# Performance work log

Measured on AMD Instinct MI355X. Metric: run time of the kernel, lower is better.

Reference implementation:

```python
import jax, jax.numpy as jnp
import numpy as np

HEADS = 16
HEAD_DIM = 64
TOKEN_DIM = 1024
INNER = HEADS * HEAD_DIM


def setup_inputs() -> dict:
    key = jax.random.key(0)
    k1, k2, k3, k4 = jax.random.split(key, 4)
    x = jax.random.normal(k1, (2, 2048, TOKEN_DIM), dtype=jnp.float32)
    # nn.Linear(token_dim, inner*3, bias=False): weight [3*inner, token_dim]
    w_qkv = jax.random.normal(k2, (3 * INNER, TOKEN_DIM), dtype=jnp.float32) * (TOKEN_DIM ** -0.5)
    # nn.Linear(inner, token_dim): weight [token_dim, inner], bias [token_dim]
    w_out = jax.random.normal(k3, (TOKEN_DIM, INNER), dtype=jnp.float32) * (INNER ** -0.5)
    b_out = jax.random.normal(k4, (TOKEN_DIM,), dtype=jnp.float32) * 0.01
    return {"x": x, "w_qkv": w_qkv, "w_out": w_out, "b_out": b_out}


def reference(x, w_qkv, w_out, b_out):
    b, n, _ = x.shape
    scale = HEAD_DIM ** -0.5
    qkv = x @ w_qkv.T                                  # [b, n, 3*inner]
    q, k, v = jnp.split(qkv, 3, axis=-1)
    def split_heads(t):
        return t.reshape(b, n, HEADS, HEAD_DIM).transpose(0, 2, 1, 3)  # [b,h,n,d]
    q, k, v = split_heads(q), split_heads(k), split_heads(v)
    dot = jnp.einsum('bhtd,bhsd->bhts', q, k) * scale  # [b,h,n,n]
    attn = jax.nn.softmax(dot, axis=-1)
    out = jnp.einsum('bhts,bhsd->bhtd', attn, v)       # [b,h,n,d]
    out = out.transpose(0, 2, 1, 3).reshape(b, n, INNER)
    return out @ w_out.T + b_out
```

## Files before the change

### kernel.cpp

```cpp
#include <hip/hip_runtime.h>
#include <hip/hip_bf16.h>

typedef short short4v __attribute__((ext_vector_type(4)));
typedef short short8 __attribute__((ext_vector_type(8)));
typedef float float4v __attribute__((ext_vector_type(4)));

#define HEADS 16
#define HDIM 64
#define TOKDIM 1024
#define SEQ 2048
#define BATCH 2
#define BH (BATCH*HEADS)
#define MROWS (BATCH*SEQ)

__device__ __forceinline__ short f2b(float f) {
    __hip_bfloat16 h = __float2bfloat16(f);
    return *reinterpret_cast<short*>(&h);
}
__device__ __forceinline__ float b2f(short s) {
    __hip_bfloat16 h;
    *reinterpret_cast<short*>(&h) = s;
    return __bfloat162float(h);
}
__device__ __forceinline__ short8 load8_f32_bf16(const float* __restrict__ p) {
    float4v a = *(const float4v*)p;
    float4v b = *(const float4v*)(p + 4);
    short8 r;
    r[0]=f2b(a[0]); r[1]=f2b(a[1]); r[2]=f2b(a[2]); r[3]=f2b(a[3]);
    r[4]=f2b(b[0]); r[5]=f2b(b[1]); r[6]=f2b(b[2]); r[7]=f2b(b[3]);
    return r;
}
__device__ __forceinline__ int packrn(float a, float b) {
    unsigned ua = __float_as_uint(a) + 0x8000u;
    unsigned ub = __float_as_uint(b) + 0x8000u;
    return (int)__builtin_amdgcn_perm(ub, ua, 0x07060302u);
}
__device__ __forceinline__ float hexp2(float x) {
    return __builtin_amdgcn_exp2f(x);
}

__device__ __forceinline__ void stage16(const void* g, void* l) {
    __builtin_amdgcn_global_load_lds((const __attribute__((address_space(1))) void*)g,
                                     (__attribute__((address_space(3))) void*)l, 16, 0, 0);
}

__global__ __launch_bounds__(256)
void cvt_bf16(const float* __restrict__ x,  short* __restrict__ xb,  int n8x,
              const float* __restrict__ wq, short* __restrict__ wqb, int n8q,
              const float* __restrict__ wo, short* __restrict__ wob, int n8o)
{
    int i = blockIdx.x*256 + threadIdx.x;
    const float* s; short* d; int off;
    if (i < n8x)                  { s = x;  d = xb;  off = i; }
    else if (i < n8x + n8q)       { s = wq; d = wqb; off = i - n8x; }
    else if (i < n8x + n8q + n8o) { s = wo; d = wob; off = i - n8x - n8q; }
    else return;
    *(short8*)&d[(size_t)off*8] = load8_f32_bf16(&s[(size_t)off*8]);
}

template<int ABF16>
__global__ __launch_bounds__(256)
void gemm_qkv(const void* __restrict__ Ap, const short* __restrict__ Wq,
              short* __restrict__ Qo, short* __restrict__ Ko, short* __restrict__ Vto)
{
    __shared__ __align__(16) short As[128*32];
    __shared__ __align__(16) short Bs[128*32];
    const int tid  = threadIdx.x;
    const int lane = tid & 63;
    const int wave = tid >> 6;
    const int wm = wave >> 1, wn = wave & 1;
    const int m0 = blockIdx.x * 128;
    const int n0 = blockIdx.y * 128;
    const int col16 = lane & 15, quad = lane >> 4;

    const int srow = lane >> 2;
    const int scol = (lane & 3) * 8;

    float4v acc[4][4];
    #pragma unroll
    for (int i=0;i<4;i++)
        #pragma unroll
        for (int j=0;j<4;j++) acc[i][j] = (float4v){0.f,0.f,0.f,0.f};

    for (int k0 = 0; k0 < TOKDIM; k0 += 32) {
        __syncthreads();
        if (ABF16) {
            const short* A = (const short*)Ap;
            #pragma unroll
            for (int j=0;j<2;++j) {
                const int rb = (wave*2 + j) * 16;
                stage16(&A[(size_t)(m0 + rb + srow)*TOKDIM + k0 + scol], &As[rb*32]);
            }
        } else {
            const float* A = (const float*)Ap;
            #pragma unroll
            for (int s=0;s<2;++s) {
                int blk = tid + s*256;
                int r = blk >> 2, kb = blk & 3;
                *(short8*)&As[r*32 + kb*8] = load8_f32_bf16(&A[(size_t)(m0+r)*TOKDIM + k0 + kb*8]);
            }
        }
        #pragma unroll
        for (int j=0;j<2;++j) {
            const int rb = (wave*2 + j) * 16;
            stage16(&Wq[(size_t)(n0 + rb + srow)*TOKDIM + k0 + scol], &Bs[rb*32]);
        }
        __syncthreads();

        short8 af[4], bfr[4];
        #pragma unroll
        for (int i=0;i<4;i++) af[i]  = *(const short8*)&As[(wm*64 + i*16 + col16)*32 + quad*8];
        #pragma unroll
        for (int j=0;j<4;j++) bfr[j] = *(const short8*)&Bs[(wn*64 + j*16 + col16)*32 + quad*8];
        #pragma unroll
        for (int i=0;i<4;i++)
            #pragma unroll
            for (int j=0;j<4;j++)
                acc[i][j] = __builtin_amdgcn_mfma_f32_16x16x32_bf16(af[i], bfr[j], acc[i][j], 0,0,0);
    }

    #pragma unroll
    for (int i=0;i<4;i++)
        #pragma unroll
        for (int j=0;j<4;j++) {
            const int n = n0 + wn*64 + j*16 + col16;
            const int part = n >> 10;
            const int h = (n & 1023) >> 6;
            const int d = n & 63;
            const int mb = m0 + wm*64 + i*16 + quad*4;
            const int b = mb >> 11;
            const int t = mb & 2047;
            if (part == 2) {
                union { short4v s; int2 i2; } w;
                #pragma unroll
                for (int r=0;r<4;r++) w.s[r] = f2b(acc[i][j][r]);
                *(int2*)&Vto[((size_t)(b*HEADS + h)*HDIM + d)*SEQ + t] = w.i2;
            } else {
                short* dst = (part == 0) ? Qo : Ko;
                #pragma unroll
                for (int r=0;r<4;r++)
                    dst[((size_t)(b*HEADS + h)*SEQ + t + r)*HDIM + d] = f2b(acc[i][j][r]);
            }
        }
}

__global__ __launch_bounds__(256)
void gemm_out(const short* __restrict__ A, const short* __restrict__ W,
              const float* __restrict__ bias, float* __restrict__ C)
{
    __shared__ __align__(16) short As[64*32];
    __shared__ __align__(16) short Bs[128*32];
    const int tid  = threadIdx.x;
    const int lane = tid & 63;
    const int wave = tid >> 6;
    const int wm = wave >> 1, wn = wave & 1;
    const int m0 = blockIdx.x * 64;
    const int n0 = blockIdx.y * 128;
    const int col16 = lane & 15, quad = lane >> 4;

    const int srow = lane >> 2;
    const int scol = (lane & 3) * 8;

    float4v acc[2][4];
    #pragma unroll
    for (int i=0;i<2;i++)
        #pragma unroll
        for (int j=0;j<4;j++) acc[i][j] = (float4v){0.f,0.f,0.f,0.f};

    for (int k0 = 0; k0 < TOKDIM; k0 += 32) {
        __syncthreads();
        {
            const int rb = wave * 16;
            stage16(&A[(size_t)(m0 + rb + srow)*TOKDIM + k0 + scol], &As[rb*32]);
        }
        #pragma unroll
        for (int j=0;j<2;++j) {
            const int rb = (wave*2 + j) * 16;
            stage16(&W[(size_t)(n0 + rb + srow)*TOKDIM + k0 + scol], &Bs[rb*32]);
        }
        __syncthreads();

        short8 af[2], bfr[4];
        #pragma unroll
        for (int i=0;i<2;i++) af[i]  = *(const short8*)&As[(wm*32 + i*16 + col16)*32 + quad*8];
        #pragma unroll
        for (int j=0;j<4;j++) bfr[j] = *(const short8*)&Bs[(wn*64 + j*16 + col16)*32 + quad*8];
        #pragma unroll
        for (int i=0;i<2;i++)
            #pragma unroll
            for (int j=0;j<4;j++)
                acc[i][j] = __builtin_amdgcn_mfma_f32_16x16x32_bf16(af[i], bfr[j], acc[i][j], 0,0,0);
    }

    #pragma unroll
    for (int i=0;i<2;i++)
        #pragma unroll
        for (int j=0;j<4;j++) {
            const int n = n0 + wn*64 + j*16 + col16;
            const float bn = bias[n];
            #pragma unroll
            for (int r=0;r<4;r++) {
                const int m = m0 + wm*32 + i*16 + quad*4 + r;
                C[(size_t)m*TOKDIM + n] = acc[i][j][r] + bn;
            }
        }
}

#define AQB 128
#define KT  64
#define NTH 16
#define KVT (KT*HDIM)
#define BUF2 (2*KVT)

__global__ __launch_bounds__(256, 2)
void attn_kernel(const short* __restrict__ Q, const short* __restrict__ K,
                 const short* __restrict__ Vt, short* __restrict__ AO)
{
    __shared__ __align__(16) short SL[2*2*BUF2];

    const int tid   = threadIdx.x;
    const int lane  = tid & 63;
    const int wave  = tid >> 6;
    const int col16 = lane & 15, quad = lane >> 4;
    const int bh  = blockIdx.y;
    const int qh  = wave & 1;
    const int kh2 = wave >> 1;
    const int qb  = blockIdx.x*AQB + qh*64;

    const short* Qb = Q  + (size_t)bh*SEQ*HDIM;
    const short* Kb = K  + (size_t)bh*SEQ*HDIM;
    const short* Vb = Vt + (size_t)bh*HDIM*SEQ;

    short* Sbase = &SL[kh2*2*BUF2];
    const int kbase = kh2 * 1024;

    const int w   = wave & 1;
    const int l3  = lane >> 3;
    const int scsw = (((lane & 7) ^ l3) << 4) >> 1;
    int krow[4], vrow[4];
    #pragma unroll
    for (int c=0;c<4;++c) {
        const int s = w*32 + c*8 + l3;
        krow[c] = (s&32) + ((s&12)<<1) + ((s&16)>>2) + (s&3);
        vrow[c] = s;
    }

    const int r7 = col16 & 7;
    int scol2[2];
    #pragma unroll
    for (int j=0;j<2;++j)
        scol2[j] = ((((j<<6) | (quad<<4)) ^ (r7<<4)) >> 1);

    const float qscale = 0.125f * 1.44269504088896f;
    short8 qf[4][2];
    #pragma unroll
    for (int qg=0; qg<4; ++qg)
        #pragma unroll
        for (int kk=0; kk<2; ++kk) {
            short8 raw = *(const short8*)&Qb[(size_t)(qb+qg*16+col16)*HDIM + kk*32 + quad*8];
            #pragma unroll
            for (int j=0;j<8;++j) raw[j] = f2b(b2f(raw[j]) * qscale);
            qf[qg][kk] = raw;
        }

    const short one_bf16 = (short)0x3F80;
    const short8 vones = {one_bf16, one_bf16, one_bf16, one_bf16,
                          one_bf16, one_bf16, one_bf16, one_bf16};

    float4v o[4][4];
    float4v o1[4];
    #pragma unroll
    for (int qg=0;qg<4;qg++) {
        #pragma unroll
        for (int dt=0;dt<4;dt++) o[qg][dt] = (float4v){0.f,0.f,0.f,0.f};
        o1[qg] = (float4v){0.f,0.f,0.f,0.f};
    }

    {
        short* Kn = Sbase;
        short* Vn = Sbase + KVT;
        #pragma unroll
        for (int c=0;c<4;++c) {
            stage16(&Kb[(size_t)(kbase + krow[c])*HDIM + scsw], &Kn[w*2048 + c*512]);
            stage16(&Vb[(size_t)vrow[c]*SEQ + kbase + scsw],    &Vn[w*2048 + c*512]);
        }
    }
    __syncthreads();

    for (int t = 0; t < NTH; ++t) {
        short* Kc = Sbase + (t & 1)*BUF2;
        short* Vc = Kc + KVT;

        if (t + 1 < NTH) {
            const int g1 = kbase + (t+1)*KT;
            short* Kn = Sbase + ((t & 1)^1)*BUF2;
            short* Vn = Kn + KVT;
            #pragma unroll
            for (int c=0;c<4;++c) {
                stage16(&Kb[(size_t)(g1 + krow[c])*HDIM + scsw], &Kn[w*2048 + c*512]);
                stage16(&Vb[(size_t)vrow[c]*SEQ + g1 + scsw],    &Vn[w*2048 + c*512]);
            }
        }

        #pragma unroll
        for (int kk = 0; kk < 2; ++kk) {
            short8 ka[2][2];
            #pragma unroll
            for (int nt=0; nt<2; ++nt)
                #pragma unroll
                for (int kh=0; kh<2; ++kh)
                    ka[nt][kh] = *(const short8*)&Kc[(kk*32 + nt*16 + col16)*64 + scol2[kh]];
            short8 va[4];
            #pragma unroll
            for (int dt=0; dt<4; ++dt)
                va[dt] = *(const short8*)&Vc[(dt*16 + col16)*64 + scol2[kk]];

            #pragma unroll
            for (int qg=0; qg<4; ++qg) {
                float4v st[2];
                __builtin_amdgcn_s_setprio(1);
                #pragma unroll
                for (int nt=0; nt<2; ++nt) {
                    float4v z = (float4v){0.f,0.f,0.f,0.f};
                    z = __builtin_amdgcn_mfma_f32_16x16x32_bf16(ka[nt][0], qf[qg][0], z, 0,0,0);
                    z = __builtin_amdgcn_mfma_f32_16x16x32_bf16(ka[nt][1], qf[qg][1], z, 0,0,0);
                    st[nt] = z;
                }
                __builtin_amdgcn_s_setprio(0);
                union { int i[4]; short8 s8; } pb;
                float p00 = hexp2(st[0][0]), p01 = hexp2(st[0][1]);
                float p02 = hexp2(st[0][2]), p03 = hexp2(st[0][3]);
                float p10 = hexp2(st[1][0]), p11 = hexp2(st[1][1]);
                float p12 = hexp2(st[1][2]), p13 = hexp2(st[1][3]);
                pb.i[0] = packrn(p00, p01); pb.i[1] = packrn(p02, p03);
                pb.i[2] = packrn(p10, p11); pb.i[3] = packrn(p12, p13);

                __builtin_amdgcn_s_setprio(1);
                #pragma unroll
                for (int dt=0; dt<4; ++dt)
                    o[qg][dt] = __builtin_amdgcn_mfma_f32_16x16x32_bf16(va[dt], pb.s8, o[qg][dt], 0,0,0);
                o1[qg] = __builtin_amdgcn_mfma_f32_16x16x32_bf16(vones, pb.s8, o1[qg], 0,0,0);
                __builtin_amdgcn_s_setprio(0);
            }
        }

        __syncthreads();
    }

    float lsum[4];
    #pragma unroll
    for (int qg=0; qg<4; ++qg) lsum[qg] = o1[qg][0];

    float* M = (float*)SL;
    float* Mw = M + (qh*64 + lane)*68;
    if (kh2 == 1) {
        #pragma unroll
        for (int qg=0; qg<4; ++qg) {
            #pragma unroll
            for (int dt=0; dt<4; ++dt)
                *(float4v*)&Mw[(qg*4+dt)*4] = o[qg][dt];
            Mw[64+qg] = lsum[qg];
        }
    }
    __syncthreads();
    if (kh2 == 0) {
        const int b = bh >> 4, h = bh & 15;
        #pragma unroll
        for (int qg=0; qg<4; ++qg) {
            lsum[qg] += Mw[64+qg];
            const float inv = 1.0f / lsum[qg];
            const int tq = qb + qg*16 + col16;
            #pragma unroll
            for (int dt=0; dt<4; ++dt) {
                float4v ov = o[qg][dt] + *(const float4v*)&Mw[(qg*4+dt)*4];
                union { short4v s; int2 i2; } w2;
                #pragma unroll
                for (int r=0;r<4;++r) w2.s[r] = f2b(ov[r] * inv);
                *(int2*)&AO[((size_t)(b*SEQ + tq))*TOKDIM + h*64 + dt*16 + quad*4] = w2.i2;
            }
        }
    }
}

extern "C" void kernel_launch(void* const* d_in, const int* in_sizes, int n_in,
                              void* d_out, int out_size, void* d_ws, size_t ws_size,
                              hipStream_t stream)
{
    const float* x    = (const float*)d_in[0];
    const float* wqkv = (const float*)d_in[1];
    const float* wout = (const float*)d_in[2];
    const float* bout = (const float*)d_in[3];
    float* out = (float*)d_out;

    char* ws = (char*)d_ws;
    const size_t SZ   = (size_t)BH*SEQ*HDIM*sizeof(short);
    const size_t WQB  = (size_t)3*TOKDIM*TOKDIM*sizeof(short);
    const size_t WOB  = (size_t)TOKDIM*TOKDIM*sizeof(short);
    const size_t NEED_FULL = SZ + WQB + WOB + 3*SZ;
    const bool full = ws_size >= NEED_FULL;

    short *Xb, *Wqb, *Wob, *Qt, *Kt, *Vt, *AO;
    if (full) {
        Xb  = (short*)ws;
        Wqb = (short*)(ws + SZ);
        Wob = (short*)(ws + SZ + WQB);
        Qt  = (short*)(ws + SZ + WQB + WOB);
        Kt  = Qt + SZ/2;
        Vt  = Kt + SZ/2;
        AO  = Xb;
    } else {
        Xb  = nullptr;
        Wqb = (short*)ws;
        Wob = (short*)(ws + WQB);
        Qt  = (short*)(ws + WQB + WOB);
        Kt  = Qt + SZ/2;
        Vt  = Kt + SZ/2;
        AO  = Vt + SZ/2;
    }

    const int n8x = full ? (BATCH*SEQ*TOKDIM)/8 : 0;
    const int n8q = (3*TOKDIM*TOKDIM)/8;
    const int n8o = (TOKDIM*TOKDIM)/8;
    const int cvt_blocks = (n8x + n8q + n8o + 255) / 256;
    cvt_bf16<<<cvt_blocks, 256, 0, stream>>>(x, Xb, n8x, wqkv, Wqb, n8q, wout, Wob, n8o);

    if (full)
        gemm_qkv<1><<<dim3(MROWS/128, (3*TOKDIM)/128), 256, 0, stream>>>(
            (const void*)Xb, Wqb, Qt, Kt, Vt);
    else
        gemm_qkv<0><<<dim3(MROWS/128, (3*TOKDIM)/128), 256, 0, stream>>>(
            (const void*)x, Wqb, Qt, Kt, Vt);

    attn_kernel<<<dim3(SEQ/AQB, BH), 256, 0, stream>>>(Qt, Kt, Vt, AO);

    gemm_out<<<dim3(MROWS/64, TOKDIM/128), 256, 0, stream>>>(AO, Wob, bout, out);
}
```

Before: 171.9 us.

## Add 256x256 double-buffered swizzled QKV GEMM with 512 threads

Replaces the 128x128, BK=32 QKV projection GEMM on the bf16 path with a 256x256 tile, BK=64 kernel using 8 waves. It double-buffers LDS so global-to-LDS loads for the next K tile overlap MFMA work, and uses an XOR swizzle to avoid LDS bank conflicts. It also raises wave priority around MFMA. The larger tile improves operand reuse, but the grid drops to 16x12=192 blocks, which may underfill the CUs, and 128KB of LDS per block limits occupancy.

```diff
diff --git a/kernel.cpp b/kernel.cpp
--- a/kernel.cpp
+++ b/kernel.cpp
@@ -58,10 +58,115 @@
     *(short8*)&d[(size_t)off*8] = load8_f32_bf16(&s[(size_t)off*8]);
 }
 
-template<int ABF16>
+#define GBM 256
+#define GBN 256
+#define GBK 64
+#define GKT (TOKDIM/GBK)
+
+__global__ __launch_bounds__(512)
+void gemm_qkv_big(const short* __restrict__ A, const short* __restrict__ Wq,
+                  short* __restrict__ Qo, short* __restrict__ Ko, short* __restrict__ Vto)
+{
+    __shared__ __align__(16) short Asl[2*GBM*GBK];
+    __shared__ __align__(16) short Bsl[2*GBN*GBK];
+
+    const int tid  = threadIdx.x;
+    const int lane = tid & 63;
+    const int wv   = tid >> 6;
+    const int wm   = wv >> 2;
+    const int wn   = wv & 3;
+    const int col16 = lane & 15, quad = lane >> 4;
+    const int m0 = blockIdx.x * GBM;
+    const int n0 = blockIdx.y * GBN;
+
+    const int srow   = lane >> 3;
+    const int scol   = (((lane & 7) ^ srow) << 3);
+
+    const int r7 = col16 & 7;
+    const int rdoff0 = (((0*4) + quad) ^ r7) << 3;
+    const int rdoff1 = (((1*4) + quad) ^ r7) << 3;
+
+    float4v acc[8][4];
+    #pragma unroll
+    for (int m=0;m<8;m++)
+        #pragma unroll
+        for (int j=0;j<4;j++) acc[m][j] = (float4v){0.f,0.f,0.f,0.f};
+
+    #pragma unroll
+    for (int c=0;c<4;++c) {
+        const int rb = (wv*4 + c)*8;
+        stage16(&A [(size_t)(m0 + rb + srow)*TOKDIM + scol], &Asl[rb*GBK]);
+        stage16(&Wq[(size_t)(n0 + rb + srow)*TOKDIM + scol], &Bsl[rb*GBK]);
+    }
+    asm volatile("s_waitcnt vmcnt(0)" ::: "memory");
+    __builtin_amdgcn_s_barrier();
+
+    for (int kt = 0; kt < GKT; ++kt) {
+        const int buf = kt & 1;
+        const short* Ab = &Asl[buf*GBM*GBK];
+        const short* Bb = &Bsl[buf*GBN*GBK];
+        short* An = &Asl[(buf^1)*GBM*GBK];
+        short* Bn = &Bsl[(buf^1)*GBN*GBK];
+        const bool more = (kt + 1 < GKT);
+        const int k1 = (kt + 1)*GBK;
+
+        #pragma unroll
+        for (int p = 0; p < 4; ++p) {
+            if (more) {
+                const int rb = (wv*4 + p)*8;
+                stage16(&A [(size_t)(m0 + rb + srow)*TOKDIM + k1 + scol], &An[rb*GBK]);
+                stage16(&Wq[(size_t)(n0 + rb + srow)*TOKDIM + k1 + scol], &Bn[rb*GBK]);
+            }
+            const int mh = p >> 1, kk = p & 1;
+            const int rdoff = kk ? rdoff1 : rdoff0;
+            short8 af[4], bfr[4];
+            #pragma unroll
+            for (int i=0;i<4;i++)
+                af[i]  = *(const short8*)&Ab[(wm*128 + mh*64 + i*16 + col16)*GBK + rdoff];
+            #pragma unroll
+            for (int j=0;j<4;j++)
+                bfr[j] = *(const short8*)&Bb[(wn*64 + j*16 + col16)*GBK + rdoff];
+            __builtin_amdgcn_s_setprio(1);
+            #pragma unroll
+            for (int i=0;i<4;i++)
+                #pragma unroll
+                for (int j=0;j<4;j++)
+                    acc[mh*4+i][j] = __builtin_amdgcn_mfma_f32_16x16x32_bf16(af[i], bfr[j], acc[mh*4+i][j], 0,0,0);
+            __builtin_amdgcn_s_setprio(0);
+        }
+
+        asm volatile("s_waitcnt vmcnt(0)" ::: "memory");
+        __builtin_amdgcn_s_barrier();
+    }
+
+    #pragma unroll
+    for (int m=0;m<8;m++)
+        #pragma unroll
+        for (int j=0;j<4;j++) {
+            const int n = n0 + wn*64 + j*16 + col16;
+            const int part = n >> 10;
+            const int h = (n & 1023) >> 6;
+            const int d = n & 63;
+            const int mb = m0 + wm*128 + m*16 + quad*4;
+            const int b = mb >> 11;
+            const int t = mb & 2047;
+            if (part == 2) {
+                union { short4v s; int2 i2; } w;
+                #pragma unroll
+                for (int r=0;r<4;r++) w.s[r] = f2b(acc[m][j][r]);
+                *(int2*)&Vto[((size_t)(b*HEADS + h)*HDIM + d)*SEQ + t] = w.i2;
+            } else {
+                short* dst = (part == 0) ? Qo : Ko;
+                #pragma unroll
+                for (int r=0;r<4;r++)
+                    dst[((size_t)(b*HEADS + h)*SEQ + t + r)*HDIM + d] = f2b(acc[m][j][r]);
+            }
+        }
+}
+
 __global__ __launch_bounds__(256)
-void gemm_qkv(const void* __restrict__ Ap, const short* __restrict__ Wq,
-              short* __restrict__ Qo, short* __restrict__ Ko, short* __restrict__ Vto)
+void gemm_qkv_small(const float* __restrict__ A, const short* __restrict__ Wq,
+                    short* __restrict__ Qo, short* __restrict__ Ko, short* __restrict__ Vto)
 {
     __shared__ __align__(16) short As[128*32];
     __shared__ __align__(16) short Bs[128*32];
@@ -84,21 +189,11 @@
 
     for (int k0 = 0; k0 < TOKDIM; k0 += 32) {
         __syncthreads();
-        if (ABF16) {
-            const short* A = (const short*)Ap;
-            #pragma unroll
-            for (int j=0;j<2;++j) {
-                const int rb = (wave*2 + j) * 16;
-                stage16(&A[(size_t)(m0 + rb + srow)*TOKDIM + k0 + scol], &As[rb*32]);
-            }
-        } else {
-            const float* A = (const float*)Ap;
-            #pragma unroll
-            for (int s=0;s<2;++s) {
-                int blk = tid + s*256;
-                int r = blk >> 2, kb = blk & 3;
-                *(short8*)&As[r*32 + kb*8] = load8_f32_bf16(&A[(size_t)(m0+r)*TOKDIM + k0 + kb*8]);
-            }
+        #pragma unroll
+        for (int s=0;s<2;++s) {
+            int blk = tid + s*256;
+            int r = blk >> 2, kb = blk & 3;
+            *(short8*)&As[r*32 + kb*8] = load8_f32_bf16(&A[(size_t)(m0+r)*TOKDIM + k0 + kb*8]);
         }
         #pragma unroll
         for (int j=0;j<2;++j) {
@@ -425,11 +520,11 @@
     cvt_bf16<<<cvt_blocks, 256, 0, stream>>>(x, Xb, n8x, wqkv, Wqb, n8q, wout, Wob, n8o);
 
     if (full)
-        gemm_qkv<1><<<dim3(MROWS/128, (3*TOKDIM)/128), 256, 0, stream>>>(
-            (const void*)Xb, Wqb, Qt, Kt, Vt);
+        gemm_qkv_big<<<dim3(MROWS/GBM, (3*TOKDIM)/GBN), 512, 0, stream>>>(
+            Xb, Wqb, Qt, Kt, Vt);
     else
-        gemm_qkv<0><<<dim3(MROWS/128, (3*TOKDIM)/128), 256, 0, stream>>>(
-            (const void*)x, Wqb, Qt, Kt, Vt);
+        gemm_qkv_small<<<dim3(MROWS/128, (3*TOKDIM)/128), 256, 0, stream>>>(
+            x, Wqb, Qt, Kt, Vt);
 
     attn_kernel<<<dim3(SEQ/AQB, BH), 256, 0, stream>>>(Qt, Kt, Vt, AO);
 
```

After: 186.3 us. 8.3% more time.

## Double-buffer output GEMM with larger K tile and XOR-swizzled LDS

Applied to the files above, without the earlier changes.

Rewrites the output projection GEMM so global-to-LDS staging of the next 64-wide K tile overlaps MFMA work on the current tile. It uses two LDS buffers, one barrier per iteration, and an XOR swizzle on LDS columns to cut bank conflicts. It also raises MFMA priority around the compute burst. The cost is doubled LDS use, which may lower occupancy, and only this one of the four kernels changes, so the gain is limited to the out-projection's share of the total time.

```diff
diff --git a/kernel.cpp b/kernel.cpp
--- a/kernel.cpp
+++ b/kernel.cpp
@@ -144,22 +144,31 @@
         }
 }
 
+#define OBM 64
+#define OBN 128
+#define OBK 64
+#define OKT (TOKDIM/OBK)
+
 __global__ __launch_bounds__(256)
 void gemm_out(const short* __restrict__ A, const short* __restrict__ W,
               const float* __restrict__ bias, float* __restrict__ C)
 {
-    __shared__ __align__(16) short As[64*32];
-    __shared__ __align__(16) short Bs[128*32];
+    __shared__ __align__(16) short Asl[2*OBM*OBK];
+    __shared__ __align__(16) short Bsl[2*OBN*OBK];
     const int tid  = threadIdx.x;
     const int lane = tid & 63;
     const int wave = tid >> 6;
     const int wm = wave >> 1, wn = wave & 1;
-    const int m0 = blockIdx.x * 64;
-    const int n0 = blockIdx.y * 128;
+    const int m0 = blockIdx.x * OBM;
+    const int n0 = blockIdx.y * OBN;
     const int col16 = lane & 15, quad = lane >> 4;
 
-    const int srow = lane >> 2;
-    const int scol = (lane & 3) * 8;
+    const int srow = lane >> 3;
+    const int scol = (((lane & 7) ^ srow) << 3);
+
+    const int r7 = col16 & 7;
+    const int rdoff0 = ((0*4 + quad) ^ r7) << 3;
+    const int rdoff1 = ((1*4 + quad) ^ r7) << 3;
 
     float4v acc[2][4];
     #pragma unroll
@@ -167,29 +176,61 @@
         #pragma unroll
         for (int j=0;j<4;j++) acc[i][j] = (float4v){0.f,0.f,0.f,0.f};
 
-    for (int k0 = 0; k0 < TOKDIM; k0 += 32) {
-        __syncthreads();
-        {
-            const int rb = wave * 16;
-            stage16(&A[(size_t)(m0 + rb + srow)*TOKDIM + k0 + scol], &As[rb*32]);
-        }
-        #pragma unroll
-        for (int j=0;j<2;++j) {
-            const int rb = (wave*2 + j) * 16;
-            stage16(&W[(size_t)(n0 + rb + srow)*TOKDIM + k0 + scol], &Bs[rb*32]);
-        }
-        __syncthreads();
-
-        short8 af[2], bfr[4];
-        #pragma unroll
-        for (int i=0;i<2;i++) af[i]  = *(const short8*)&As[(wm*32 + i*16 + col16)*32 + quad*8];
-        #pragma unroll
-        for (int j=0;j<4;j++) bfr[j] = *(const short8*)&Bs[(wn*64 + j*16 + col16)*32 + quad*8];
-        #pragma unroll
-        for (int i=0;i<2;i++)
+    #pragma unroll
+    for (int c=0;c<2;++c) {
+        const int rb = (wave*2 + c)*8;
+        stage16(&A[(size_t)(m0 + rb + srow)*TOKDIM + scol], &Asl[rb*OBK]);
+    }
+    #pragma unroll
+    for (int c=0;c<4;++c) {
+        const int rb = (wave*4 + c)*8;
+        stage16(&W[(size_t)(n0 + rb + srow)*TOKDIM + scol], &Bsl[rb*OBK]);
+    }
+    asm volatile("s_waitcnt vmcnt(0)" ::: "memory");
+    __builtin_amdgcn_s_barrier();
+
+    for (int kt = 0; kt < OKT; ++kt) {
+        const int buf = kt & 1;
+        const short* Ab = &Asl[buf*OBM*OBK];
+        const short* Bb = &Bsl[buf*OBN*OBK];
+        short* An = &Asl[(buf^1)*OBM*OBK];
+        short* Bn = &Bsl[(buf^1)*OBN*OBK];
+
+        if (kt + 1 < OKT) {
+            const int k1 = (kt + 1)*OBK;
+            #pragma unroll
+            for (int c=0;c<2;++c) {
+                const int rb = (wave*2 + c)*8;
+                stage16(&A[(size_t)(m0 + rb + srow)*TOKDIM + k1 + scol], &An[rb*OBK]);
+            }
+            #pragma unroll
+            for (int c=0;c<4;++c) {
+                const int rb = (wave*4 + c)*8;
+                stage16(&W[(size_t)(n0 + rb + srow)*TOKDIM + k1 + scol], &Bn[rb*OBK]);
+            }
+        }
+
+        #pragma unroll
+        for (int kk=0;kk<2;++kk) {
+            const int rdoff = kk ? rdoff1 : rdoff0;
+            short8 af[2], bfr[4];
+            #pragma unroll
+            for (int i=0;i<2;i++)
+                af[i]  = *(const short8*)&Ab[(wm*32 + i*16 + col16)*OBK + rdoff];
             #pragma unroll
             for (int j=0;j<4;j++)
-                acc[i][j] = __builtin_amdgcn_mfma_f32_16x16x32_bf16(af[i], bfr[j], acc[i][j], 0,0,0);
+                bfr[j] = *(const short8*)&Bb[(wn*64 + j*16 + col16)*OBK + rdoff];
+            __builtin_amdgcn_s_setprio(1);
+            #pragma unroll
+            for (int i=0;i<2;i++)
+                #pragma unroll
+                for (int j=0;j<4;j++)
+                    acc[i][j] = __builtin_amdgcn_mfma_f32_16x16x32_bf16(af[i], bfr[j], acc[i][j], 0,0,0);
+            __builtin_amdgcn_s_setprio(0);
+        }
+
+        asm volatile("s_waitcnt vmcnt(0)" ::: "memory");
+        __builtin_amdgcn_s_barrier();
     }
 
     #pragma unroll
@@ -433,5 +474,5 @@
 
     attn_kernel<<<dim3(SEQ/AQB, BH), 256, 0, stream>>>(Qt, Kt, Vt, AO);
 
-    gemm_out<<<dim3(MROWS/64, TOKDIM/128), 256, 0, stream>>>(AO, Wob, bout, out);
-}
+    gemm_out<<<dim3(MROWS/OBM, TOKDIM/OBN), 256, 0, stream>>>(AO, Wob, bout, out);
+}
```

Result: no change. 170.1 us (median of 2 runs) (-1.1%).
